# Optimization experiments

Hardware: AMD Instinct MI355X
Metric: run time of the kernel (lower is better)

## Reference

```python
import jax, jax.numpy as jnp
import numpy as np


def _conv(x, w, b, pad):
    # x: (B,C,H,W), w: (O,I,kh,kw), NCHW conv with given padding
    y = jax.lax.conv_general_dilated(x, w, window_strides=(1, 1), padding=pad,
                                     dimension_numbers=('NCHW', 'OIHW', 'NCHW'))
    return y + b[None, :, None, None]


def _frn(x, eps):
    # FilterResponseNorm: normalize by rms over spatial dims (2,3)
    nu2 = jnp.mean(x * x, axis=(2, 3), keepdims=True)
    return x * jax.lax.rsqrt(nu2 + jnp.abs(eps))


def _mish(x):
    return x * jnp.tanh(jax.nn.softplus(x))


def setup_inputs() -> dict:
    key = jax.random.key(0)
    ks = jax.random.split(key, 9)
    B, C, H, W = 4, 256, 64, 64
    C16 = C // 16
    x = jax.random.normal(ks[0], (B, C, H, W), dtype=jnp.float32)
    s = 0.05
    wq = jax.random.normal(ks[1], (C16, C, 1, 3), dtype=jnp.float32) * s
    bq = jax.random.normal(ks[2], (C16,), dtype=jnp.float32) * s
    wk = jax.random.normal(ks[3], (C16, C, 3, 1), dtype=jnp.float32) * s
    bk = jax.random.normal(ks[4], (C16,), dtype=jnp.float32) * s
    wv = jax.random.normal(ks[5], (C, C, 1, 1), dtype=jnp.float32) * s
    bv = jax.random.normal(ks[6], (C,), dtype=jnp.float32) * s
    gamma = jax.random.normal(ks[7], (1,), dtype=jnp.float32) * 0.1
    eps_q = jnp.full((1, C16, 1, 1), 1e-6, dtype=jnp.float32)
    eps_k = jnp.full((1, C16, 1, 1), 1e-6, dtype=jnp.float32)
    return {"x": x, "wq": wq, "bq": bq, "wk": wk, "bk": bk,
            "wv": wv, "bv": bv, "gamma": gamma, "eps_q": eps_q, "eps_k": eps_k}


def reference(x, wq, bq, wk, bk, wv, bv, gamma, eps_q, eps_k):
    B, C, H, W = x.shape
    N = H * W
    # query branch: Conv2d(k=(1,3), pad=(0,1)) -> FRN -> Mish
    q = _mish(_frn(_conv(x, wq, bq, [(0, 0), (1, 1)]), eps_q))  # (B,C16,H,W)
    # key branch: Conv2d(k=(3,1), pad=(1,0)) -> FRN -> Mish
    k = _mish(_frn(_conv(x, wk, bk, [(1, 1), (0, 0)]), eps_k))  # (B,C16,H,W)
    q = q.reshape(B, -1, N)  # (B,C16,N)
    k = k.reshape(B, -1, N)  # (B,C16,N)
    # affinity[b,n,m] = sum_c q[b,c,n] * k[b,c,m]; softmax over m
    affinity = jnp.einsum('bcn,bcm->bnm', q, k)
    affinity = jax.nn.softmax(affinity, axis=-1)  # (B,N,N)
    v = _conv(x, wv, bv, [(0, 0), (0, 0)]).reshape(B, C, N)  # (B,C,N)
    # weights = v @ affinity^T : weights[b,c,j] = sum_n v[b,c,n] * affinity[b,j,n]
    weights = jnp.einsum('bcn,bjn->bcj', v, affinity).reshape(B, C, H, W)
    return gamma * weights + x
```

## Files before the change

### kernel.cpp

```cpp
#include <hip/hip_runtime.h>
#include <stdint.h>

#define NB 4
#define CC 256
#define C16 16
#define HH 64
#define WW 64
#define NN 4096

typedef __attribute__((ext_vector_type(8))) short short8;
typedef __attribute__((ext_vector_type(4))) float floatx4;
typedef __attribute__((ext_vector_type(16))) float floatx16;

#if __has_builtin(__builtin_amdgcn_exp2f)
#define EXP2(x) __builtin_amdgcn_exp2f(x)
#else
#define EXP2(x) exp2f(x)
#endif

__device__ __forceinline__ unsigned short f2bf(float f) {
    union { float f; unsigned u; } v; v.f = f;
    unsigned r = v.u + 0x7fffu + ((v.u >> 16) & 1u);
    return (unsigned short)(r >> 16);
}
__device__ __forceinline__ float bf2f(unsigned short h) {
    union { unsigned u; float f; } v; v.u = (unsigned)h << 16;
    return v.f;
}



__device__ __forceinline__ void prep_tile_body(
        int vb, const float* __restrict__ x, unsigned short* __restrict__ xT,
        float (*tile_t)[65], int tid) {
    int nt = vb & 63, ct = (vb >> 6) & 3, b = vb >> 8;
    int n0 = nt * 64, c0 = ct * 64;
    int rg = tid >> 4, f = tid & 15;
    const float* xb = x + ((size_t)b * CC + c0) * NN + n0;
#pragma unroll
    for (int p = 0; p < 4; ++p) {
        int c = p * 16 + rg;
        float4 v = *(const float4*)(xb + (size_t)c * NN + f * 4);
        tile_t[f * 4 + 0][c] = v.x;
        tile_t[f * 4 + 1][c] = v.y;
        tile_t[f * 4 + 2][c] = v.z;
        tile_t[f * 4 + 3][c] = v.w;
    }
    __syncthreads();
    unsigned short* xtb = xT + ((size_t)b * NN + n0) * CC + c0;
#pragma unroll
    for (int p = 0; p < 4; ++p) {
        int n = p * 16 + rg;
        ushort4 st;
        st.x = f2bf(tile_t[n][f * 4 + 0]);
        st.y = f2bf(tile_t[n][f * 4 + 1]);
        st.z = f2bf(tile_t[n][f * 4 + 2]);
        st.w = f2bf(tile_t[n][f * 4 + 3]);
        *(ushort4*)(xtb + (size_t)n * CC + f * 4) = st;
    }
}

__device__ __forceinline__ void prep_wt_body(
        int vb, const float* __restrict__ wv, const float* __restrict__ wq,
        const float* __restrict__ wk, unsigned short* __restrict__ wvb,
        unsigned short* __restrict__ wqkb, float* __restrict__ nu2, int tid) {
    int idx = (vb - 1024) * 256 + tid;
    if (vb == 1024 && tid < 128) nu2[tid] = 0.f;
    if (idx < 16384) {
        float4 v = *(const float4*)(wv + idx * 4);
        ushort4 o;
        o.x = f2bf(v.x); o.y = f2bf(v.y); o.z = f2bf(v.z); o.w = f2bf(v.w);
        *(ushort4*)(wvb + idx * 4) = o;
    } else if (idx < 16384 + 6144) {
        int base = (idx - 16384) * 4;
#pragma unroll
        for (int u = 0; u < 4; ++u) {
            int e = base + u;
            int t = e / 12288;
            int i = e - t * 12288;
            int tap = i >> 12, o = (i >> 8) & 15, c = i & 255;
            const float* src = t ? wk : wq;
            wqkb[e] = f2bf(src[o * 768 + c * 3 + tap]);
        }
    }
}

__device__ __forceinline__ void conv_v_body(
        int vb, const unsigned short* __restrict__ xT, const unsigned short* __restrict__ wvb,
        const float* __restrict__ bv, unsigned short* __restrict__ vbuf, int tid) {
    int wv_ = tid >> 6, lane = tid & 63;
    int q16 = lane >> 4, c16 = lane & 15;
    int ntile = vb & 63, b = (vb >> 6) & 3, ch = vb >> 8;
    int n0 = ntile * 64;
    int cb = ch * 128 + wv_ * 32;
    floatx4 fzero = {0.f, 0.f, 0.f, 0.f};
    floatx4 acc[2][4];
    for (int ct = 0; ct < 2; ++ct)
        for (int nt = 0; nt < 4; ++nt) acc[ct][nt] = fzero;
    const unsigned short* xb = xT + ((size_t)b * NN + n0) * CC;
    for (int kc = 0; kc < 8; ++kc) {
        int ko = kc * 32 + q16 * 8;
        short8 a0 = *(const short8*)(wvb + (size_t)(cb + c16) * CC + ko);
        short8 a1 = *(const short8*)(wvb + (size_t)(cb + 16 + c16) * CC + ko);
        short8 bf[4];
#pragma unroll
        for (int nt = 0; nt < 4; ++nt)
            bf[nt] = *(const short8*)(xb + (size_t)(nt * 16 + c16) * CC + ko);
#pragma unroll
        for (int nt = 0; nt < 4; ++nt) {
            acc[0][nt] = __builtin_amdgcn_mfma_f32_16x16x32_bf16(bf[nt], a0, acc[0][nt], 0, 0, 0);
            acc[1][nt] = __builtin_amdgcn_mfma_f32_16x16x32_bf16(bf[nt], a1, acc[1][nt], 0, 0, 0);
        }
    }
    float bv0 = bv[cb + c16], bv1 = bv[cb + 16 + c16];
    int off = 32 * 8 * (q16 >> 1) + (q16 & 1) * 4 + c16 * 8;
#pragma unroll
    for (int ct = 0; ct < 2; ++ct) {
        float bvv = ct ? bv1 : bv0;
#pragma unroll
        for (int nt = 0; nt < 4; ++nt) {
            size_t fb = (((size_t)b * 8 + ch * 4 + wv_) * 256 + (n0 >> 4) + nt) * 512;
            ushort4 st;
            st.x = f2bf(acc[ct][nt][0] + bvv);
            st.y = f2bf(acc[ct][nt][1] + bvv);
            st.z = f2bf(acc[ct][nt][2] + bvv);
            st.w = f2bf(acc[ct][nt][3] + bvv);
            *(ushort4*)(vbuf + fb + off + ct * 16 * 8) = st;
        }
    }
}

__device__ __forceinline__ void conv_qk_body_v2(
        int u, const unsigned short* __restrict__ xT, const unsigned short* __restrict__ wqkb,
        const float* __restrict__ bq, const float* __restrict__ bk,
        unsigned short* __restrict__ qrawh, unsigned short* __restrict__ krawh,
        float* __restrict__ nu2, int tid,
        float4 (*redq)[64], float4 (*redk)[64]) {
    int w = tid >> 6, lane = tid & 63;
    int q16 = lane >> 4, c16 = lane & 15;
    int b = u >> 8, unit = u & 255;
    int n0 = unit * 16;
    int nl = n0 + c16;
    int hh = nl >> 6, ww = nl & 63;
    bool vm1 = (ww != 0), vp1 = (ww != 63);
    bool vm64 = (hh != 0), vp64 = (hh != 63);
    short8 zero8 = {0, 0, 0, 0, 0, 0, 0, 0};
    floatx4 accq = {0.f, 0.f, 0.f, 0.f}, acck = {0.f, 0.f, 0.f, 0.f};
    const unsigned short* xb = xT + (size_t)b * NN * CC;
    const unsigned short* wrow = wqkb + c16 * 256;
#pragma unroll
    for (int kk = 0; kk < 2; ++kk) {
        int kc = w * 2 + kk;
        int ko = kc * 32 + q16 * 8;
        short8 b0 = *(const short8*)(xb + (size_t)nl * CC + ko);
        short8 bm1 = vm1 ? *(const short8*)(xb + (size_t)(nl - 1) * CC + ko) : zero8;
        short8 bp1 = vp1 ? *(const short8*)(xb + (size_t)(nl + 1) * CC + ko) : zero8;
        short8 bm64 = vm64 ? *(const short8*)(xb + (size_t)(nl - 64) * CC + ko) : zero8;
        short8 bp64 = vp64 ? *(const short8*)(xb + (size_t)(nl + 64) * CC + ko) : zero8;
        short8 aq0 = *(const short8*)(wrow + 0 * 4096 + ko);
        short8 aq1 = *(const short8*)(wrow + 1 * 4096 + ko);
        short8 aq2 = *(const short8*)(wrow + 2 * 4096 + ko);
        short8 ak0 = *(const short8*)(wrow + 12288 + 0 * 4096 + ko);
        short8 ak1 = *(const short8*)(wrow + 12288 + 1 * 4096 + ko);
        short8 ak2 = *(const short8*)(wrow + 12288 + 2 * 4096 + ko);
        accq = __builtin_amdgcn_mfma_f32_16x16x32_bf16(bm1, aq0, accq, 0, 0, 0);
        accq = __builtin_amdgcn_mfma_f32_16x16x32_bf16(b0, aq1, accq, 0, 0, 0);
        accq = __builtin_amdgcn_mfma_f32_16x16x32_bf16(bp1, aq2, accq, 0, 0, 0);
        acck = __builtin_amdgcn_mfma_f32_16x16x32_bf16(bm64, ak0, acck, 0, 0, 0);
        acck = __builtin_amdgcn_mfma_f32_16x16x32_bf16(b0, ak1, acck, 0, 0, 0);
        acck = __builtin_amdgcn_mfma_f32_16x16x32_bf16(bp64, ak2, acck, 0, 0, 0);
    }
    float4 pq, pk;
    pq.x = accq[0]; pq.y = accq[1]; pq.z = accq[2]; pq.w = accq[3];
    pk.x = acck[0]; pk.y = acck[1]; pk.z = acck[2]; pk.w = acck[3];
    redq[w][lane] = pq;
    redk[w][lane] = pk;
    __syncthreads();
    if (w == 0) {
        float4 a0 = redq[0][lane], a1 = redq[1][lane], a2 = redq[2][lane], a3 = redq[3][lane];
        float s0 = ((a0.x + a1.x) + a2.x) + a3.x;
        float s1 = ((a0.y + a1.y) + a2.y) + a3.y;
        float s2 = ((a0.z + a1.z) + a2.z) + a3.z;
        float s3 = ((a0.w + a1.w) + a2.w) + a3.w;
        float bqv = bq[c16];
        float vq0 = s0 + bqv, vq1 = s1 + bqv, vq2 = s2 + bqv, vq3 = s3 + bqv;
        ushort4 sq4;
        sq4.x = f2bf(vq0); sq4.y = f2bf(vq1); sq4.z = f2bf(vq2); sq4.w = f2bf(vq3);
        *(ushort4*)(qrawh + (size_t)(b * C16 + c16) * NN + n0 + q16 * 4) = sq4;
        float ssq = vq0 * vq0 + vq1 * vq1 + vq2 * vq2 + vq3 * vq3;
        ssq += __shfl_xor(ssq, 16, 64);
        ssq += __shfl_xor(ssq, 32, 64);
        if (lane < 16) atomicAdd(nu2 + b * C16 + lane, ssq);
    } else if (w == 1) {
        float4 a0 = redk[0][lane], a1 = redk[1][lane], a2 = redk[2][lane], a3 = redk[3][lane];
        float s0 = ((a0.x + a1.x) + a2.x) + a3.x;
        float s1 = ((a0.y + a1.y) + a2.y) + a3.y;
        float s2 = ((a0.z + a1.z) + a2.z) + a3.z;
        float s3 = ((a0.w + a1.w) + a2.w) + a3.w;
        float bkv = bk[c16];
        float vk0 = s0 + bkv, vk1 = s1 + bkv, vk2 = s2 + bkv, vk3 = s3 + bkv;
        ushort4 sk4;
        sk4.x = f2bf(vk0); sk4.y = f2bf(vk1); sk4.z = f2bf(vk2); sk4.w = f2bf(vk3);
        *(ushort4*)(krawh + (size_t)(b * C16 + c16) * NN + n0 + q16 * 4) = sk4;
        float ssk = vk0 * vk0 + vk1 * vk1 + vk2 * vk2 + vk3 * vk3;
        ssk += __shfl_xor(ssk, 16, 64);
        ssk += __shfl_xor(ssk, 32, 64);
        if (lane < 16) atomicAdd(nu2 + 64 + b * C16 + lane, ssk);
    }
}

__device__ __forceinline__ void frn_body(
        int blk, const unsigned short* __restrict__ qrawh, const unsigned short* __restrict__ krawh,
        const float* __restrict__ nu2, const float* __restrict__ eps_q,
        const float* __restrict__ eps_k, unsigned short* __restrict__ qb,
        unsigned short* __restrict__ kb, int tid) {
    int tensor = blk >> 8;
    int b = (blk >> 6) & 3;
    int nch = blk & 63;
    const unsigned short* raw = tensor ? krawh : qrawh;
    const float* eps = tensor ? eps_k : eps_q;
    unsigned short* outp = tensor ? kb : qb;
    const float* nu = nu2 + tensor * 64 + b * C16;
    float scale = tensor ? 1.0f : 1.44269504f;
    int n = nch * 64 + (tid & 63);
    int oq = tid >> 6;
    ushort4 pk4;
#pragma unroll
    for (int i = 0; i < 4; ++i) {
        int o = oq * 4 + i;
        float r = bf2f(raw[(size_t)(b * C16 + o) * NN + n]);
        float v = r * rsqrtf(nu[o] * (1.f / (float)NN) + fabsf(eps[o]));
        float t = EXP2(v * 1.44269504f);
        float num = t * t + 2.0f * t;
        float m = (v * num) * __builtin_amdgcn_rcpf(num + 2.0f);
        if (v > 30.f) m = v;
        m *= scale;
        ((unsigned short*)&pk4)[i] = f2bf(m);
    }
    size_t base = ((size_t)b * 128 + (n >> 5)) * 512 + (size_t)(n & 31) * 8
                + (size_t)(oq >> 1) * 256 + (oq & 1) * 4;
    *(ushort4*)(outp + base) = pk4;
}

__device__ __forceinline__ void pack_half(
        const floatx16& sc, int h, short8* A, float* lsum) {
    unsigned pk[4];
    float ls = 0.f;
#pragma unroll
    for (int p = 0; p < 4; ++p) {
        float e0 = EXP2(sc[8 * h + 2 * p]);
        float e1 = EXP2(sc[8 * h + 2 * p + 1]);
        ls += e0 + e1;
        pk[p] = __builtin_amdgcn_perm(__float_as_uint(e1), __float_as_uint(e0), 0x07060302u);
    }
    *lsum += ls;
    asm("v_permlane32_swap_b32 %0, %1" : "+v"(pk[0]), "+v"(pk[2]));
    asm("v_permlane32_swap_b32 %0, %1" : "+v"(pk[1]), "+v"(pk[3]));
    union { unsigned u[4]; short8 s; } a;
    a.u[0] = pk[0]; a.u[1] = pk[1]; a.u[2] = pk[2]; a.u[3] = pk[3];
    *A = a.s;
}

__device__ __forceinline__ void attn_body(
        int id, const unsigned short* __restrict__ qb, const unsigned short* __restrict__ kb,
        const unsigned short* __restrict__ vbuf, const float* __restrict__ x,
        const float* __restrict__ gamma_p, float* __restrict__ out,
        float (*lpart)[2][32], float (*obuf)[32][33], int tid) {
    int wv_ = __builtin_amdgcn_readfirstlane(tid >> 6);
    int lane = tid & 63;
    int l31 = lane & 31, lh = lane >> 5;
    int cs = id & 1, b = (id >> 1) & 3, jt = id >> 3;
    int jbase = jt * 64, cb = cs * 128;
    int lane8 = lane * 8;

    const unsigned short* qfb = qb + ((size_t)b * 128 + (jbase >> 5)) * 512 + lane8;
    const unsigned short* kfb = kb + ((size_t)b * 128 + (wv_ * 32)) * 512 + lane8;

    short8 qf0 = *(const short8*)qfb;
    short8 qf1 = *(const short8*)(qfb + 512);

    floatx16 z16 = {0,0,0,0,0,0,0,0,0,0,0,0,0,0,0,0};
    floatx16 acc0[4], acc1[4];
#pragma unroll
    for (int cg = 0; cg < 4; ++cg) { acc0[cg] = z16; acc1[cg] = z16; }
    float lsum0 = 0.f, lsum1 = 0.f;

    const unsigned short* vp0 = vbuf + (((size_t)b * 8 + cs * 4 + 0) * 256 + wv_ * 64) * 512 + lane8;
    const unsigned short* vp1 = vbuf + (((size_t)b * 8 + cs * 4 + 1) * 256 + wv_ * 64) * 512 + lane8;
    const unsigned short* vp2 = vbuf + (((size_t)b * 8 + cs * 4 + 2) * 256 + wv_ * 64) * 512 + lane8;
    const unsigned short* vp3 = vbuf + (((size_t)b * 8 + cs * 4 + 3) * 256 + wv_ * 64) * 512 + lane8;

    short8 ak = *(const short8*)kfb;
#pragma unroll 1
    for (int step = 0; step < 32; ++step) {
        short8 vf0a = *(const short8*)vp0;
        short8 vf1a = *(const short8*)vp1;
        short8 vf2a = *(const short8*)vp2;
        short8 vf3a = *(const short8*)vp3;
        short8 vf0b = *(const short8*)(vp0 + 512);
        short8 vf1b = *(const short8*)(vp1 + 512);
        short8 vf2b = *(const short8*)(vp2 + 512);
        short8 vf3b = *(const short8*)(vp3 + 512);
        floatx16 sc0 = __builtin_amdgcn_mfma_f32_32x32x16_bf16(ak, qf0, z16, 0, 0, 0);
        floatx16 sc1 = __builtin_amdgcn_mfma_f32_32x32x16_bf16(ak, qf1, z16, 0, 0, 0);
        ak = *(const short8*)(kfb + (size_t)((step + 1) & 31) * 512);
        short8 A;
        pack_half(sc0, 0, &A, &lsum0);
        __builtin_amdgcn_s_setprio(1);
        acc0[0] = __builtin_amdgcn_mfma_f32_32x32x16_bf16(A, vf0a, acc0[0], 0, 0, 0);
        acc0[1] = __builtin_amdgcn_mfma_f32_32x32x16_bf16(A, vf1a, acc0[1], 0, 0, 0);
        acc0[2] = __builtin_amdgcn_mfma_f32_32x32x16_bf16(A, vf2a, acc0[2], 0, 0, 0);
        acc0[3] = __builtin_amdgcn_mfma_f32_32x32x16_bf16(A, vf3a, acc0[3], 0, 0, 0);
        __builtin_amdgcn_s_setprio(0);
        __builtin_amdgcn_sched_barrier(0);
        pack_half(sc0, 1, &A, &lsum0);
        __builtin_amdgcn_s_setprio(1);
        acc0[0] = __builtin_amdgcn_mfma_f32_32x32x16_bf16(A, vf0b, acc0[0], 0, 0, 0);
        acc0[1] = __builtin_amdgcn_mfma_f32_32x32x16_bf16(A, vf1b, acc0[1], 0, 0, 0);
        acc0[2] = __builtin_amdgcn_mfma_f32_32x32x16_bf16(A, vf2b, acc0[2], 0, 0, 0);
        acc0[3] = __builtin_amdgcn_mfma_f32_32x32x16_bf16(A, vf3b, acc0[3], 0, 0, 0);
        __builtin_amdgcn_s_setprio(0);
        __builtin_amdgcn_sched_barrier(0);
        pack_half(sc1, 0, &A, &lsum1);
        __builtin_amdgcn_s_setprio(1);
        acc1[0] = __builtin_amdgcn_mfma_f32_32x32x16_bf16(A, vf0a, acc1[0], 0, 0, 0);
        acc1[1] = __builtin_amdgcn_mfma_f32_32x32x16_bf16(A, vf1a, acc1[1], 0, 0, 0);
        acc1[2] = __builtin_amdgcn_mfma_f32_32x32x16_bf16(A, vf2a, acc1[2], 0, 0, 0);
        acc1[3] = __builtin_amdgcn_mfma_f32_32x32x16_bf16(A, vf3a, acc1[3], 0, 0, 0);
        __builtin_amdgcn_s_setprio(0);
        __builtin_amdgcn_sched_barrier(0);
        pack_half(sc1, 1, &A, &lsum1);
        __builtin_amdgcn_s_setprio(1);
        acc1[0] = __builtin_amdgcn_mfma_f32_32x32x16_bf16(A, vf0b, acc1[0], 0, 0, 0);
        acc1[1] = __builtin_amdgcn_mfma_f32_32x32x16_bf16(A, vf1b, acc1[1], 0, 0, 0);
        acc1[2] = __builtin_amdgcn_mfma_f32_32x32x16_bf16(A, vf2b, acc1[2], 0, 0, 0);
        acc1[3] = __builtin_amdgcn_mfma_f32_32x32x16_bf16(A, vf3b, acc1[3], 0, 0, 0);
        __builtin_amdgcn_s_setprio(0);
        vp0 += 1024; vp1 += 1024; vp2 += 1024; vp3 += 1024;
    }

    lsum0 += __shfl_xor(lsum0, 32, 64);
    lsum1 += __shfl_xor(lsum1, 32, 64);
    if (lh == 0) { lpart[wv_][0][l31] = lsum0; lpart[wv_][1][l31] = lsum1; }
    __syncthreads();

    int j31 = tid & 31;
    float gamma = gamma_p[0];
    float gl0 = gamma / (lpart[0][0][j31] + lpart[1][0][j31] + lpart[2][0][j31] + lpart[3][0][j31]);
    float gl1 = gamma / (lpart[0][1][j31] + lpart[1][1][j31] + lpart[2][1][j31] + lpart[3][1][j31]);
    const float* xbb = x + (size_t)b * CC * NN;
    float* obb = out + (size_t)b * CC * NN;
    int hofs = lh * 4;
    int cgrp = tid >> 5;
#pragma unroll
    for (int jg = 0; jg < 2; ++jg) {
        float gl = jg ? gl1 : gl0;
#pragma unroll
        for (int cg = 0; cg < 4; ++cg) {
            __syncthreads();
            const floatx16& a = jg ? acc1[cg] : acc0[cg];
#pragma unroll
            for (int r = 0; r < 16; ++r) {
                int row = (r & 3) + 8 * (r >> 2) + hofs;
                obuf[wv_][row][l31] = a[r];
            }
            __syncthreads();
#pragma unroll
            for (int i = 0; i < 4; ++i) {
                int c = cgrp * 4 + i;
                float val = obuf[0][j31][c] + obuf[1][j31][c] + obuf[2][j31][c] + obuf[3][j31][c];
                size_t oidx = (size_t)(cb + cg * 32 + c) * NN + jbase + jg * 32 + j31;
                obb[oidx] = fmaf(gl, val, xbb[oidx]);
            }
        }
    }
}

__global__ __launch_bounds__(256) void prep_kernel(
        const float* __restrict__ x, const float* __restrict__ wv,
        const float* __restrict__ wq, const float* __restrict__ wk,
        unsigned short* __restrict__ xT, unsigned short* __restrict__ wvb,
        unsigned short* __restrict__ wqkb, float* __restrict__ nu2) {
    __shared__ float tile_t[64][65];
    int bid = blockIdx.x;
    if (bid < 1024) prep_tile_body(bid, x, xT, tile_t, threadIdx.x);
    else prep_wt_body(bid, wv, wq, wk, wvb, wqkb, nu2, threadIdx.x);
}

__global__ __launch_bounds__(256) void conv_kernel(
        const unsigned short* __restrict__ xT, const unsigned short* __restrict__ wvb,
        const unsigned short* __restrict__ wqkb, const float* __restrict__ bv,
        const float* __restrict__ bq, const float* __restrict__ bk,
        unsigned short* __restrict__ vbuf, unsigned short* __restrict__ qrawh,
        unsigned short* __restrict__ krawh, float* __restrict__ nu2) {
    __shared__ float4 redq[4][64];
    __shared__ float4 redk[4][64];
    int bid = blockIdx.x;
    if (bid < 512) conv_v_body(bid, xT, wvb, bv, vbuf, threadIdx.x);
    else conv_qk_body_v2(bid - 512, xT, wqkb, bq, bk, qrawh, krawh, nu2,
                         threadIdx.x, redq, redk);
}

__global__ __launch_bounds__(256) void frn_mish_kernel(
        const unsigned short* __restrict__ qrawh, const unsigned short* __restrict__ krawh,
        const float* __restrict__ nu2, const float* __restrict__ eps_q,
        const float* __restrict__ eps_k, unsigned short* __restrict__ qb,
        unsigned short* __restrict__ kb) {
    frn_body(blockIdx.x, qrawh, krawh, nu2, eps_q, eps_k, qb, kb, threadIdx.x);
}

__global__ __launch_bounds__(256, 2) void attn_kernel(
        const unsigned short* __restrict__ qb, const unsigned short* __restrict__ kb,
        const unsigned short* __restrict__ vbuf, const float* __restrict__ x,
        const float* __restrict__ gamma_p, float* __restrict__ out) {
    __shared__ float lpart[4][2][32];
    __shared__ float obuf[4][32][33];
    attn_body(blockIdx.x, qb, kb, vbuf, x, gamma_p, out, lpart, obuf, threadIdx.x);
}

extern "C" void kernel_launch(void* const* d_in, const int* in_sizes, int n_in,
                              void* d_out, int out_size, void* d_ws, size_t ws_size,
                              hipStream_t stream) {
    const float* x     = (const float*)d_in[0];
    const float* wq    = (const float*)d_in[1];
    const float* bq    = (const float*)d_in[2];
    const float* wk    = (const float*)d_in[3];
    const float* bk    = (const float*)d_in[4];
    const float* wv    = (const float*)d_in[5];
    const float* bv    = (const float*)d_in[6];
    const float* gamma = (const float*)d_in[7];
    const float* eps_q = (const float*)d_in[8];
    const float* eps_k = (const float*)d_in[9];
    float* out = (float*)d_out;
    char* ws = (char*)d_ws;

    unsigned short* qrawh = (unsigned short*)ws;
    unsigned short* krawh = (unsigned short*)(ws + (1u << 20));
    float* nu2  = (float*)(ws + (2u << 20));
    unsigned short* qb = (unsigned short*)(ws + (2u << 20) + 4096);
    unsigned short* kb = qb + (size_t)NB * NN * C16;
    unsigned short* vbuf = kb + (size_t)NB * NN * C16;
    unsigned short* xT = vbuf + (size_t)NB * CC * NN;
    unsigned short* wvb = xT + (size_t)NB * NN * CC;
    unsigned short* wqkb = wvb + (size_t)CC * CC;

    prep_kernel<<<dim3(1112), dim3(256), 0, stream>>>(x, wv, wq, wk, xT, wvb, wqkb, nu2);
    conv_kernel<<<dim3(1536), dim3(256), 0, stream>>>(xT, wvb, wqkb, bv, bq, bk, vbuf, qrawh, krawh, nu2);
    frn_mish_kernel<<<dim3(512), dim3(256), 0, stream>>>(qrawh, krawh, nu2, eps_q, eps_k, qb, kb);
    attn_kernel<<<dim3(512), dim3(256), 0, stream>>>(qb, kb, vbuf, x, gamma, out);
}
```

Baseline: 159.7 us.

## Block bf16 x and weight buffers into 32-channel chunks for contiguous MFMA loads

Changes the transposed bf16 activation buffer and the converted weight buffers from row-major [n][256] layout to a blocked [kchunk][n][32] layout. Each 16-lane group's short8 loads in the conv kernels then read contiguous 64-byte rows instead of rows strided by 512 bytes, which should improve cache-line utilisation and coalescing. The prep kernel's stores become more scattered, and every consumer of xT, wvb and wqkb has to agree on the new indexing.

Measured after the change: 151.7 us (median of 2 runs). -5.0%, faster.

```diff
diff --git a/kernel.cpp b/kernel.cpp
--- a/kernel.cpp
+++ b/kernel.cpp
@@ -47,7 +47,7 @@
         tile_t[f * 4 + 3][c] = v.w;
     }
     __syncthreads();
-    unsigned short* xtb = xT + ((size_t)b * NN + n0) * CC + c0;
+    unsigned short* xtb = xT + (((size_t)b * 8 + ct * 2 + (f >> 3)) * NN + n0) * 32 + (f & 7) * 4;
 #pragma unroll
     for (int p = 0; p < 4; ++p) {
         int n = p * 16 + rg;
@@ -56,7 +56,7 @@
         st.y = f2bf(tile_t[n][f * 4 + 1]);
         st.z = f2bf(tile_t[n][f * 4 + 2]);
         st.w = f2bf(tile_t[n][f * 4 + 3]);
-        *(ushort4*)(xtb + (size_t)n * CC + f * 4) = st;
+        *(ushort4*)(xtb + (size_t)n * 32) = st;
     }
 }
 
@@ -70,7 +70,9 @@
         float4 v = *(const float4*)(wv + idx * 4);
         ushort4 o;
         o.x = f2bf(v.x); o.y = f2bf(v.y); o.z = f2bf(v.z); o.w = f2bf(v.w);
-        *(ushort4*)(wvb + idx * 4) = o;
+        int e0 = idx * 4;
+        int co = e0 >> 8, c = e0 & 255;
+        *(ushort4*)(wvb + ((size_t)(c >> 5) * 256 + co) * 32 + (c & 31)) = o;
     } else if (idx < 16384 + 6144) {
         int base = (idx - 16384) * 4;
 #pragma unroll
@@ -80,7 +82,8 @@
             int i = e - t * 12288;
             int tap = i >> 12, o = (i >> 8) & 15, c = i & 255;
             const float* src = t ? wk : wq;
-            wqkb[e] = f2bf(src[o * 768 + c * 3 + tap]);
+            wqkb[(((size_t)(t * 3 + tap) * 8 + (c >> 5)) * 16 + o) * 32 + (c & 31)]
+                = f2bf(src[o * 768 + c * 3 + tap]);
         }
     }
 }
@@ -97,15 +100,16 @@
     floatx4 acc[2][4];
     for (int ct = 0; ct < 2; ++ct)
         for (int nt = 0; nt < 4; ++nt) acc[ct][nt] = fzero;
-    const unsigned short* xb = xT + ((size_t)b * NN + n0) * CC;
+    int lo8 = q16 * 8;
     for (int kc = 0; kc < 8; ++kc) {
-        int ko = kc * 32 + q16 * 8;
-        short8 a0 = *(const short8*)(wvb + (size_t)(cb + c16) * CC + ko);
-        short8 a1 = *(const short8*)(wvb + (size_t)(cb + 16 + c16) * CC + ko);
+        const unsigned short* xk = xT + (((size_t)b * 8 + kc) * NN + n0) * 32;
+        const unsigned short* wk_ = wvb + ((size_t)kc * 256 + cb) * 32;
+        short8 a0 = *(const short8*)(wk_ + c16 * 32 + lo8);
+        short8 a1 = *(const short8*)(wk_ + (16 + c16) * 32 + lo8);
         short8 bf[4];
 #pragma unroll
         for (int nt = 0; nt < 4; ++nt)
-            bf[nt] = *(const short8*)(xb + (size_t)(nt * 16 + c16) * CC + ko);
+            bf[nt] = *(const short8*)(xk + (nt * 16 + c16) * 32 + lo8);
 #pragma unroll
         for (int nt = 0; nt < 4; ++nt) {
             acc[0][nt] = __builtin_amdgcn_mfma_f32_16x16x32_bf16(bf[nt], a0, acc[0][nt], 0, 0, 0);
@@ -146,23 +150,23 @@
     bool vm64 = (hh != 0), vp64 = (hh != 63);
     short8 zero8 = {0, 0, 0, 0, 0, 0, 0, 0};
     floatx4 accq = {0.f, 0.f, 0.f, 0.f}, acck = {0.f, 0.f, 0.f, 0.f};
-    const unsigned short* xb = xT + (size_t)b * NN * CC;
-    const unsigned short* wrow = wqkb + c16 * 256;
+    int lo8 = q16 * 8;
 #pragma unroll
     for (int kk = 0; kk < 2; ++kk) {
         int kc = w * 2 + kk;
-        int ko = kc * 32 + q16 * 8;
-        short8 b0 = *(const short8*)(xb + (size_t)nl * CC + ko);
-        short8 bm1 = vm1 ? *(const short8*)(xb + (size_t)(nl - 1) * CC + ko) : zero8;
-        short8 bp1 = vp1 ? *(const short8*)(xb + (size_t)(nl + 1) * CC + ko) : zero8;
-        short8 bm64 = vm64 ? *(const short8*)(xb + (size_t)(nl - 64) * CC + ko) : zero8;
-        short8 bp64 = vp64 ? *(const short8*)(xb + (size_t)(nl + 64) * CC + ko) : zero8;
-        short8 aq0 = *(const short8*)(wrow + 0 * 4096 + ko);
-        short8 aq1 = *(const short8*)(wrow + 1 * 4096 + ko);
-        short8 aq2 = *(const short8*)(wrow + 2 * 4096 + ko);
-        short8 ak0 = *(const short8*)(wrow + 12288 + 0 * 4096 + ko);
-        short8 ak1 = *(const short8*)(wrow + 12288 + 1 * 4096 + ko);
-        short8 ak2 = *(const short8*)(wrow + 12288 + 2 * 4096 + ko);
+        const unsigned short* xk = xT + (((size_t)b * 8 + kc) * NN) * 32;
+        short8 b0 = *(const short8*)(xk + (size_t)nl * 32 + lo8);
+        short8 bm1 = vm1 ? *(const short8*)(xk + (size_t)(nl - 1) * 32 + lo8) : zero8;
+        short8 bp1 = vp1 ? *(const short8*)(xk + (size_t)(nl + 1) * 32 + lo8) : zero8;
+        short8 bm64 = vm64 ? *(const short8*)(xk + (size_t)(nl - 64) * 32 + lo8) : zero8;
+        short8 bp64 = vp64 ? *(const short8*)(xk + (size_t)(nl + 64) * 32 + lo8) : zero8;
+        int wbase = kc * 512 + c16 * 32 + lo8;
+        short8 aq0 = *(const short8*)(wqkb + 0 * 4096 + wbase);
+        short8 aq1 = *(const short8*)(wqkb + 1 * 4096 + wbase);
+        short8 aq2 = *(const short8*)(wqkb + 2 * 4096 + wbase);
+        short8 ak0 = *(const short8*)(wqkb + 12288 + 0 * 4096 + wbase);
+        short8 ak1 = *(const short8*)(wqkb + 12288 + 1 * 4096 + wbase);
+        short8 ak2 = *(const short8*)(wqkb + 12288 + 2 * 4096 + wbase);
         accq = __builtin_amdgcn_mfma_f32_16x16x32_bf16(bm1, aq0, accq, 0, 0, 0);
         accq = __builtin_amdgcn_mfma_f32_16x16x32_bf16(b0, aq1, accq, 0, 0, 0);
         accq = __builtin_amdgcn_mfma_f32_16x16x32_bf16(bp1, aq2, accq, 0, 0, 0);
```
